# Kernel tuning notes

Hardware: AMD Instinct MI355X
Metric: run time of the kernel (lower is better)

The kernel has to match this reference:

```python
import jax, jax.numpy as jnp
import numpy as np

TAU_PRE = 2.0
TAU_POST = 2.0
KH, KW = 3, 3
B, CIN, H, W = 16, 64, 66, 66
COUT = 128
HOUT, WOUT = H - KH + 1, W - KW + 1  # stride 1, padding 0


def setup_inputs() -> dict:
    key = jax.random.key(0)
    k1, k2, k3, k4, k5 = jax.random.split(key, 5)
    in_spike = jax.random.uniform(k1, (B, CIN, H, W), dtype=jnp.float32)
    out_spike = jax.random.uniform(k2, (B, COUT, HOUT, WOUT), dtype=jnp.float32)
    trace_pre = jax.random.uniform(k3, (B, CIN, H, W), dtype=jnp.float32)
    trace_post = jax.random.uniform(k4, (B, COUT, HOUT, WOUT), dtype=jnp.float32)
    weight = jax.random.normal(k5, (COUT, CIN, KH, KW), dtype=jnp.float32) * 0.05
    return {"in_spike": in_spike, "out_spike": out_spike,
            "trace_pre": trace_pre, "trace_post": trace_post, "weight": weight}


def reference(in_spike, out_spike, trace_pre, trace_post, weight):
    # Trace decay + spike accumulation (faithful to torch: tr - tr/tau + spike)
    tr_pre = trace_pre - trace_pre / TAU_PRE + in_spike    # [B,Cin,H,W]
    tr_post = trace_post - trace_post / TAU_POST + out_spike  # [B,Cout,Hout,Wout]

    rows = []
    for h in range(KH):
        cols = []
        for w in range(KW):
            pre = in_spike[:, :, h:h + HOUT, w:w + WOUT]   # [B,Cin,Hout,Wout]
            trp = tr_pre[:, :, h:h + HOUT, w:w + WOUT]     # [B,Cin,Hout,Wout]
            wk = weight[:, :, h, w]                        # [Cout,Cin]
            # sum over batch and spatial dims of outer products
            s_pre = jnp.einsum('bopq,bipq->oi', tr_post, pre)      # [Cout,Cin]
            s_post = jnp.einsum('bipq,bopq->oi', trp, out_spike)   # [Cout,Cin]
            cols.append(-wk * s_pre + wk * s_post)
        rows.append(jnp.stack(cols, axis=-1))  # [Cout,Cin,KW]
    delta_w = jnp.stack(rows, axis=-2)          # [Cout,Cin,KH,KW]
    return tr_pre, tr_post, delta_w
```

## Files before the change

kernel.cpp:

```cpp
#include <hip/hip_runtime.h>


typedef unsigned short ushort_t;
typedef unsigned int uint_t;
typedef __attribute__((ext_vector_type(8))) short short8;
typedef __attribute__((ext_vector_type(4))) float floatx4;
typedef __attribute__((ext_vector_type(2))) float floatx2;
typedef __attribute__((ext_vector_type(4))) int intx4;
typedef __attribute__((ext_vector_type(4))) uint_t uintx4;

#define N_POST   8388608
#define N_DW     73728
#define O_TRPOST 4460544
#define O_DW     12849152

#define MFMA_BLOCKS  384
#define FILLA_BLOCKS 1024
#define FILLB_BLOCKS 768
#define TOTAL_BLOCKS 2176
#define B_ROWS_PER_WAVE 22

__device__ __forceinline__ int cvt2bf(float lo, float hi) {
  int r; asm("v_cvt_pk_bf16_f32 %0, %1, %2" : "=v"(r) : "v"(lo), "v"(hi)); return r;
}
__device__ __forceinline__ int cvt2bfn(float lo, float hi) {
  int r; asm("v_cvt_pk_bf16_f32 %0, -%1, -%2" : "=v"(r) : "v"(lo), "v"(hi)); return r;
}
__device__ __forceinline__ int bsh2(int hi, int lo) {
  return (int)((((unsigned long long)(uint_t)hi << 32) | (uint_t)lo) >> 16);
}

__global__ __launch_bounds__(256, 2)
void k_main(const float* __restrict__ in_sp, const float* __restrict__ out_sp,
            const float* __restrict__ tpre, const float* __restrict__ tpost,
            float* __restrict__ o_trpre, float* __restrict__ o_trpost,
            float* __restrict__ partials, int use_ws) {
  const int bx0 = blockIdx.x;
  const int t = threadIdx.x;

  if (bx0 >= MFMA_BLOCKS) {
    if (bx0 < MFMA_BLOCKS + FILLA_BLOCKS) {
      int i4 = (bx0 - MFMA_BLOCKS) * 256 + t;
      #pragma unroll
      for (int it = 0; it < 8; ++it, i4 += FILLA_BLOCKS * 256) {
        floatx4 o = __builtin_nontemporal_load((const floatx4*)(out_sp + i4 * 4));
        floatx4 p = __builtin_nontemporal_load((const floatx4*)(tpost + i4 * 4));
        floatx4 v = 0.5f * p + o;
        __builtin_nontemporal_store(v, (floatx4*)(o_trpost + i4 * 4));
      }
    } else {
      const int l = t & 63;
      if (l >= 33) return;
      const int wid = (bx0 - (MFMA_BLOCKS + FILLA_BLOCKS)) * 4 + (t >> 6);
      #pragma unroll 2
      for (int it = 0; it < B_ROWS_PER_WAVE; ++it) {
        const int g = (wid * B_ROWS_PER_WAVE + it) * 66 + l * 2;
        floatx2 a = __builtin_nontemporal_load((const floatx2*)(tpre + g));
        floatx2 c = __builtin_nontemporal_load((const floatx2*)(in_sp + g));
        floatx2 v = { 0.5f * a.x + c.x, 0.5f * a.y + c.y };
        __builtin_nontemporal_store(v, (floatx2*)(o_trpre + g));
      }
    }
    return;
  }
  if (!use_ws) return;

  __shared__ short LB[2][9728];
  const int kh = bx0 >> 7, bx = bx0 & 127;
  const int b = bx >> 3, p0 = (bx & 7) * 8;
  const int w = t >> 6, l = t & 63;
  const int quad = l >> 4, l16 = l & 15;
  const int si = t >> 2, sg = t & 3;

  const float* arow0 = out_sp + ((b * 128 + w * 32 + l16) * 4096 + quad * 8 + p0 * 64);
  const float* arow1 = tpost  + ((b * 128 + w * 32 + l16) * 4096 + quad * 8 + p0 * 64);
  const float* brow0 = tpre  + ((b * 64 + si) * 4356 + sg * 16);
  const float* brow1 = in_sp + ((b * 64 + si) * 4356 + sg * 16);
  short* Lrow = &LB[0][0] + si * 152 + sg * 16;

  floatx4 acc[3][2][4] = {};

  auto stageB = [&](int h, int buf) {
    const float* r0 = brow0 + h * 66;
    const float* r1 = brow1 + h * 66;
    floatx2 v0[8], v1[8];
    #pragma unroll
    for (int k = 0; k < 8; ++k) {
      v0[k] = *(const floatx2*)(r0 + 2 * k);
      v1[k] = *(const floatx2*)(r1 + 2 * k);
    }
    uintx4 u0a = { (uint_t)cvt2bf(v0[0].x, v0[0].y), (uint_t)cvt2bf(v0[1].x, v0[1].y),
                   (uint_t)cvt2bf(v0[2].x, v0[2].y), (uint_t)cvt2bf(v0[3].x, v0[3].y) };
    uintx4 u0b = { (uint_t)cvt2bf(v0[4].x, v0[4].y), (uint_t)cvt2bf(v0[5].x, v0[5].y),
                   (uint_t)cvt2bf(v0[6].x, v0[6].y), (uint_t)cvt2bf(v0[7].x, v0[7].y) };
    uintx4 u1a = { (uint_t)cvt2bf(v1[0].x, v1[0].y), (uint_t)cvt2bf(v1[1].x, v1[1].y),
                   (uint_t)cvt2bf(v1[2].x, v1[2].y), (uint_t)cvt2bf(v1[3].x, v1[3].y) };
    uintx4 u1b = { (uint_t)cvt2bf(v1[4].x, v1[4].y), (uint_t)cvt2bf(v1[5].x, v1[5].y),
                   (uint_t)cvt2bf(v1[6].x, v1[6].y), (uint_t)cvt2bf(v1[7].x, v1[7].y) };
    short* Lb = Lrow + buf * 9728;
    *(uintx4*)(Lb)      = u0a;
    *(uintx4*)(Lb + 8)  = u0b;
    *(uintx4*)(Lb + 72) = u1a;
    *(uintx4*)(Lb + 80) = u1b;
    if (sg == 3) {
      floatx2 t0 = *(const floatx2*)(r0 + 16);
      floatx2 t1 = *(const floatx2*)(r1 + 16);
      *(uint_t*)(Lb + 16) = (uint_t)cvt2bf(t0.x, t0.y);
      *(uint_t*)(Lb + 88) = (uint_t)cvt2bf(t1.x, t1.y);
    }
  };

  stageB(p0 + kh, 0);
  __syncthreads();

  for (int rr = 0; rr < 8; ++rr) {
    floatx4 ar[2][2][2][2];
    #pragma unroll
    for (int mt = 0; mt < 2; ++mt)
      #pragma unroll
      for (int ks = 0; ks < 2; ++ks)
        #pragma unroll
        for (int hf = 0; hf < 2; ++hf) {
          const int off = rr * 64 + mt * 65536 + ks * 32 + hf * 4;
          ar[0][mt][ks][hf] = *(const floatx4*)(arow0 + off);
          ar[1][mt][ks][hf] = *(const floatx4*)(arow1 + off);
        }
    if (rr < 7) stageB(p0 + rr + 1 + kh, (rr + 1) & 1);

    const short* Lbb = &LB[0][0] + (rr & 1) * 9728;
    #pragma unroll
    for (int ks = 0; ks < 2; ++ks) {
      short8 fa[2][2];
      #pragma unroll
      for (int mt = 0; mt < 2; ++mt) {
        uintx4 ua = { (uint_t)cvt2bf (ar[0][mt][ks][0].x, ar[0][mt][ks][0].y),
                      (uint_t)cvt2bf (ar[0][mt][ks][0].z, ar[0][mt][ks][0].w),
                      (uint_t)cvt2bf (ar[0][mt][ks][1].x, ar[0][mt][ks][1].y),
                      (uint_t)cvt2bf (ar[0][mt][ks][1].z, ar[0][mt][ks][1].w) };
        uintx4 un = { (uint_t)cvt2bfn(ar[1][mt][ks][0].x, ar[1][mt][ks][0].y),
                      (uint_t)cvt2bfn(ar[1][mt][ks][0].z, ar[1][mt][ks][0].w),
                      (uint_t)cvt2bfn(ar[1][mt][ks][1].x, ar[1][mt][ks][1].y),
                      (uint_t)cvt2bfn(ar[1][mt][ks][1].z, ar[1][mt][ks][1].w) };
        fa[0][mt] = __builtin_bit_cast(short8, ua);
        fa[1][mt] = __builtin_bit_cast(short8, un);
      }
      #pragma unroll
      for (int nt = 0; nt < 4; ++nt) {
        const int i = nt * 16 + l16;
        short8 fb[2][3];
        #pragma unroll
        for (int mat = 0; mat < 2; ++mat) {
          const int base = i * 152 + mat * 72 + ks * 32 + quad * 8;
          intx4 W = *(const intx4*)&Lbb[base];
          int W4 = *(const int*)&Lbb[base + 8];
          intx4 f0 = { W.x, W.y, W.z, W.w };
          intx4 f1 = { bsh2(W.y, W.x), bsh2(W.z, W.y), bsh2(W.w, W.z), bsh2(W4, W.w) };
          intx4 f2 = { W.y, W.z, W.w, W4 };
          fb[mat][0] = __builtin_bit_cast(short8, f0);
          fb[mat][1] = __builtin_bit_cast(short8, f1);
          fb[mat][2] = __builtin_bit_cast(short8, f2);
        }
        #pragma unroll
        for (int kw = 0; kw < 3; ++kw)
          #pragma unroll
          for (int mt = 0; mt < 2; ++mt) {
            acc[kw][mt][nt] = __builtin_amdgcn_mfma_f32_16x16x32_bf16(fa[0][mt], fb[0][kw], acc[kw][mt][nt], 0, 0, 0);
            acc[kw][mt][nt] = __builtin_amdgcn_mfma_f32_16x16x32_bf16(fa[1][mt], fb[1][kw], acc[kw][mt][nt], 0, 0, 0);
          }
      }
    }
    __syncthreads();
  }

  #pragma unroll
  for (int kw = 0; kw < 3; ++kw) {
    float* slice = partials + (size_t)((kh * 3 + kw) * 128 + bx) * 8192;
    #pragma unroll
    for (int mt = 0; mt < 2; ++mt)
      #pragma unroll
      for (int nt = 0; nt < 4; ++nt)
        #pragma unroll
        for (int rg = 0; rg < 4; ++rg) {
          const int o = w * 32 + mt * 16 + quad * 4 + rg;
          const int i = nt * 16 + l16;
          slice[o * 64 + i] = acc[kw][mt][nt][rg];
        }
  }
}

__global__ void k_finalize(const float* __restrict__ partials,
                           const float* __restrict__ weight, float* __restrict__ dw) {
  int tid = blockIdx.x * 256 + threadIdx.x;
  int e = tid >> 13, oi = tid & 8191;
  float s = 0.f;
  #pragma unroll 8
  for (int c = 0; c < 128; ++c)
    s += __builtin_nontemporal_load(partials + (size_t)(e * 128 + c) * 8192 + oi);
  int o = oi >> 6, i = oi & 63;
  int wi = (o * 64 + i) * 9 + e;
  dw[wi] = 0.5f * weight[wi] * s;
}

__global__ void k_naive(const float* __restrict__ out_sp, const float* __restrict__ tpost,
                        const float* __restrict__ tpre, const float* __restrict__ in_sp,
                        const float* __restrict__ weight, float* __restrict__ dw) {
  int tid = blockIdx.x * 256 + threadIdx.x;
  int e = tid >> 13, oi = tid & 8191;
  int o = oi >> 6, i = oi & 63;
  int kh = e / 3, kw = e - kh * 3;
  float acc = 0.f;
  for (int b = 0; b < 16; ++b)
    for (int p = 0; p < 64; ++p) {
      const float* ga = out_sp + ((b * 128 + o) * 64 + p) * 64;
      const float* gn = tpost + ((b * 128 + o) * 64 + p) * 64;
      const float* gb = tpre + ((b * 64 + i) * 66 + p + kh) * 66 + kw;
      const float* gm = in_sp + ((b * 64 + i) * 66 + p + kh) * 66 + kw;
      for (int q = 0; q < 64; ++q) acc += ga[q] * gb[q] - gn[q] * gm[q];
    }
  int wi = (o * 64 + i) * 9 + kh * 3 + kw;
  dw[wi] = 0.5f * weight[wi] * acc;
}

extern "C" void kernel_launch(void* const* d_in, const int* in_sizes, int n_in,
                              void* d_out, int out_size, void* d_ws, size_t ws_size,
                              hipStream_t stream) {
  const float* in_sp  = (const float*)d_in[0];
  const float* out_sp = (const float*)d_in[1];
  const float* tpre   = (const float*)d_in[2];
  const float* tpost  = (const float*)d_in[3];
  const float* weight = (const float*)d_in[4];
  float* out = (float*)d_out;
  float* o_trpre  = out;
  float* o_trpost = out + O_TRPOST;
  float* o_dw     = out + O_DW;

  const size_t WS_NEED = (size_t)9 * 128 * 8192 * 4;
  const int use_mfma = (ws_size >= WS_NEED) ? 1 : 0;
  float* partials = (float*)d_ws;

  k_main<<<TOTAL_BLOCKS, 256, 0, stream>>>(in_sp, out_sp, tpre, tpost,
                                           o_trpre, o_trpost, partials, use_mfma);
  if (use_mfma) {
    k_finalize<<<N_DW / 256, 256, 0, stream>>>(partials, weight, o_dw);
  } else {
    k_naive<<<N_DW / 256, 256, 0, stream>>>(out_sp, tpost, tpre, in_sp, weight, o_dw);
  }
}
```

Before: 204.2 us.

## Fuse trace updates into MFMA blocks that already load the same data

Drops the separate fill blocks that streamed out_spike/trace_post and in_spike/trace_pre a second time. The MFMA blocks now write tr_post from their A-operand registers (only kh==0 blocks) and tr_pre from their staged B rows (kh==0 blocks plus the last rows for other kh). The aim is to avoid re-reading roughly 50MB of input. In exchange the MFMA blocks carry extra store traffic on their critical path and the grid shrinks to 384 blocks, so the elementwise work is spread over fewer CUs. The partial-sum reads in finalize also drop their nontemporal hint.

```diff
diff --git a/kernel.cpp b/kernel.cpp
--- a/kernel.cpp
+++ b/kernel.cpp
@@ -15,9 +15,8 @@
 #define O_DW     12849152
 
 #define MFMA_BLOCKS  384
-#define FILLA_BLOCKS 1024
-#define FILLB_BLOCKS 768
-#define TOTAL_BLOCKS 2176
+#define FB_FILLA 1024
+#define FB_FILLB 768
 #define B_ROWS_PER_WAVE 22
 
 __device__ __forceinline__ int cvt2bf(float lo, float hi) {
@@ -34,48 +33,26 @@
 void k_main(const float* __restrict__ in_sp, const float* __restrict__ out_sp,
             const float* __restrict__ tpre, const float* __restrict__ tpost,
             float* __restrict__ o_trpre, float* __restrict__ o_trpost,
-            float* __restrict__ partials, int use_ws) {
+            float* __restrict__ partials) {
+  __shared__ short LB[2][9728];
   const int bx0 = blockIdx.x;
   const int t = threadIdx.x;
-
-  if (bx0 >= MFMA_BLOCKS) {
-    if (bx0 < MFMA_BLOCKS + FILLA_BLOCKS) {
-      int i4 = (bx0 - MFMA_BLOCKS) * 256 + t;
-      #pragma unroll
-      for (int it = 0; it < 8; ++it, i4 += FILLA_BLOCKS * 256) {
-        floatx4 o = __builtin_nontemporal_load((const floatx4*)(out_sp + i4 * 4));
-        floatx4 p = __builtin_nontemporal_load((const floatx4*)(tpost + i4 * 4));
-        floatx4 v = 0.5f * p + o;
-        __builtin_nontemporal_store(v, (floatx4*)(o_trpost + i4 * 4));
-      }
-    } else {
-      const int l = t & 63;
-      if (l >= 33) return;
-      const int wid = (bx0 - (MFMA_BLOCKS + FILLA_BLOCKS)) * 4 + (t >> 6);
-      #pragma unroll 2
-      for (int it = 0; it < B_ROWS_PER_WAVE; ++it) {
-        const int g = (wid * B_ROWS_PER_WAVE + it) * 66 + l * 2;
-        floatx2 a = __builtin_nontemporal_load((const floatx2*)(tpre + g));
-        floatx2 c = __builtin_nontemporal_load((const floatx2*)(in_sp + g));
-        floatx2 v = { 0.5f * a.x + c.x, 0.5f * a.y + c.y };
-        __builtin_nontemporal_store(v, (floatx2*)(o_trpre + g));
-      }
-    }
-    return;
-  }
-  if (!use_ws) return;
-
-  __shared__ short LB[2][9728];
   const int kh = bx0 >> 7, bx = bx0 & 127;
   const int b = bx >> 3, p0 = (bx & 7) * 8;
   const int w = t >> 6, l = t & 63;
   const int quad = l >> 4, l16 = l & 15;
   const int si = t >> 2, sg = t & 3;
 
-  const float* arow0 = out_sp + ((b * 128 + w * 32 + l16) * 4096 + quad * 8 + p0 * 64);
-  const float* arow1 = tpost  + ((b * 128 + w * 32 + l16) * 4096 + quad * 8 + p0 * 64);
-  const float* brow0 = tpre  + ((b * 64 + si) * 4356 + sg * 16);
-  const float* brow1 = in_sp + ((b * 64 + si) * 4356 + sg * 16);
+  const size_t abase = ((size_t)(b * 128 + w * 32 + l16)) * 4096 + quad * 8 + p0 * 64;
+  const float* arow0 = out_sp + abase;
+  const float* arow1 = tpost  + abase;
+  float*       otp   = o_trpost + abase;
+  const int wpost = (kh == 0);
+
+  const size_t bbase = ((size_t)(b * 64 + si)) * 4356 + sg * 16;
+  const float* brow0 = tpre  + bbase;
+  const float* brow1 = in_sp + bbase;
+  float*       opre0 = o_trpre + bbase;
   short* Lrow = &LB[0][0] + si * 152 + sg * 16;
 
   floatx4 acc[3][2][4] = {};
@@ -83,11 +60,20 @@
   auto stageB = [&](int h, int buf) {
     const float* r0 = brow0 + h * 66;
     const float* r1 = brow1 + h * 66;
+    const bool wp = (kh == 0) || (h == 63 + kh);
+    float* opre = opre0 + h * 66;
     floatx2 v0[8], v1[8];
     #pragma unroll
     for (int k = 0; k < 8; ++k) {
       v0[k] = *(const floatx2*)(r0 + 2 * k);
       v1[k] = *(const floatx2*)(r1 + 2 * k);
+    }
+    if (wp) {
+      #pragma unroll
+      for (int k = 0; k < 8; ++k) {
+        floatx2 v = { 0.5f * v0[k].x + v1[k].x, 0.5f * v0[k].y + v1[k].y };
+        *(floatx2*)(opre + 2 * k) = v;
+      }
     }
     uintx4 u0a = { (uint_t)cvt2bf(v0[0].x, v0[0].y), (uint_t)cvt2bf(v0[1].x, v0[1].y),
                    (uint_t)cvt2bf(v0[2].x, v0[2].y), (uint_t)cvt2bf(v0[3].x, v0[3].y) };
@@ -107,6 +93,10 @@
       floatx2 t1 = *(const floatx2*)(r1 + 16);
       *(uint_t*)(Lb + 16) = (uint_t)cvt2bf(t0.x, t0.y);
       *(uint_t*)(Lb + 88) = (uint_t)cvt2bf(t1.x, t1.y);
+      if (wp) {
+        floatx2 v = { 0.5f * t0.x + t1.x, 0.5f * t0.y + t1.y };
+        *(floatx2*)(opre + 16) = v;
+      }
     }
   };
 
@@ -125,6 +115,18 @@
           ar[0][mt][ks][hf] = *(const floatx4*)(arow0 + off);
           ar[1][mt][ks][hf] = *(const floatx4*)(arow1 + off);
         }
+    if (wpost) {
+      #pragma unroll
+      for (int mt = 0; mt < 2; ++mt)
+        #pragma unroll
+        for (int ks = 0; ks < 2; ++ks)
+          #pragma unroll
+          for (int hf = 0; hf < 2; ++hf) {
+            const int off = rr * 64 + mt * 65536 + ks * 32 + hf * 4;
+            floatx4 v = 0.5f * ar[1][mt][ks][hf] + ar[0][mt][ks][hf];
+            *(floatx4*)(otp + off) = v;
+          }
+    }
     if (rr < 7) stageB(p0 + rr + 1 + kh, (rr + 1) & 1);
 
     const short* Lbb = &LB[0][0] + (rr & 1) * 9728;
@@ -194,11 +196,39 @@
   int e = tid >> 13, oi = tid & 8191;
   float s = 0.f;
   #pragma unroll 8
-  for (int c = 0; c < 128; ++c)
-    s += __builtin_nontemporal_load(partials + (size_t)(e * 128 + c) * 8192 + oi);
+  for (int c = 0; c < 128; ++c) s += partials[(size_t)(e * 128 + c) * 8192 + oi];
   int o = oi >> 6, i = oi & 63;
   int wi = (o * 64 + i) * 9 + e;
   dw[wi] = 0.5f * weight[wi] * s;
+}
+
+__global__ __launch_bounds__(256)
+void k_fill_fb(const float* __restrict__ in_sp, const float* __restrict__ out_sp,
+               const float* __restrict__ tpre, const float* __restrict__ tpost,
+               float* __restrict__ o_trpre, float* __restrict__ o_trpost) {
+  const int bx = blockIdx.x;
+  const int t = threadIdx.x;
+  if (bx < FB_FILLA) {
+    int i4 = bx * 256 + t;
+    #pragma unroll
+    for (int it = 0; it < 8; ++it, i4 += FB_FILLA * 256) {
+      floatx4 o = *(const floatx4*)(out_sp + i4 * 4);
+      floatx4 p = *(const floatx4*)(tpost + i4 * 4);
+      *(floatx4*)(o_trpost + i4 * 4) = 0.5f * p + o;
+    }
+  } else {
+    const int l = t & 63;
+    if (l >= 33) return;
+    const int wid = (bx - FB_FILLA) * 4 + (t >> 6);
+    #pragma unroll 2
+    for (int it = 0; it < B_ROWS_PER_WAVE; ++it) {
+      const int g = (wid * B_ROWS_PER_WAVE + it) * 66 + l * 2;
+      floatx2 a = *(const floatx2*)(tpre + g);
+      floatx2 c = *(const floatx2*)(in_sp + g);
+      floatx2 v = { 0.5f * a.x + c.x, 0.5f * a.y + c.y };
+      *(floatx2*)(o_trpre + g) = v;
+    }
+  }
 }
 
 __global__ void k_naive(const float* __restrict__ out_sp, const float* __restrict__ tpost,
@@ -238,11 +268,13 @@
   const int use_mfma = (ws_size >= WS_NEED) ? 1 : 0;
   float* partials = (float*)d_ws;
 
-  k_main<<<TOTAL_BLOCKS, 256, 0, stream>>>(in_sp, out_sp, tpre, tpost,
-                                           o_trpre, o_trpost, partials, use_mfma);
   if (use_mfma) {
+    k_main<<<MFMA_BLOCKS, 256, 0, stream>>>(in_sp, out_sp, tpre, tpost,
+                                            o_trpre, o_trpost, partials);
     k_finalize<<<N_DW / 256, 256, 0, stream>>>(partials, weight, o_dw);
   } else {
+    k_fill_fb<<<FB_FILLA + FB_FILLB, 256, 0, stream>>>(in_sp, out_sp, tpre, tpost,
+                                                       o_trpre, o_trpost);
     k_naive<<<N_DW / 256, 256, 0, stream>>>(out_sp, tpost, tpre, in_sp, weight, o_dw);
   }
 }
```

Result: slower. 208.9 us (+2.3%).
